# Optimization experiments

Measured on AMD Instinct MI355X. Metric: run time of the kernel, lower is better.

The kernel has to match this reference:

```python
import jax, jax.numpy as jnp
import numpy as np

D_IN = 1024
D_OUT = 1024

def setup_inputs() -> dict:
    key = jax.random.key(0)
    ks = jax.random.split(key, 7)
    s = 1.0 / np.sqrt(D_IN)
    x = jax.random.normal(ks[0], (4, 2048, D_IN), dtype=jnp.float32)
    Wq = jax.random.uniform(ks[1], (D_IN, D_OUT), jnp.float32, -s, s)
    Wk = jax.random.uniform(ks[2], (D_IN, D_OUT), jnp.float32, -s, s)
    Wv = jax.random.uniform(ks[3], (D_IN, D_OUT), jnp.float32, -s, s)
    bq = jax.random.uniform(ks[4], (D_OUT,), jnp.float32, -s, s)
    bk = jax.random.uniform(ks[5], (D_OUT,), jnp.float32, -s, s)
    bv = jax.random.uniform(ks[6], (D_OUT,), jnp.float32, -s, s)
    return {"x": x, "Wq": Wq, "Wk": Wk, "Wv": Wv, "bq": bq, "bk": bk, "bv": bv}

def reference(x, Wq, Wk, Wv, bq, bk, bv):
    # x: [b, n, d_in]
    q = jnp.einsum('bnd,de->bne', x, Wq) + bq
    k = jnp.einsum('bnd,de->bne', x, Wk) + bk
    v = jnp.einsum('bnd,de->bne', x, Wv) + bv
    scale = 1.0 / jnp.sqrt(jnp.asarray(k.shape[-1], dtype=x.dtype))
    scores = jnp.einsum('bqe,bke->bqk', q, k) * scale  # [b, n, n]
    weights = jax.nn.softmax(scores, axis=-1)
    return jnp.einsum('bqk,bke->bqe', weights, v)
```

## Files before the change

kernel.cpp:

```cpp
#include <hip/hip_runtime.h>
#include <cstdint>

typedef __bf16 bf16x8 __attribute__((ext_vector_type(8)));
typedef float f32x16 __attribute__((ext_vector_type(16)));

__device__ __forceinline__ unsigned short f2b(float f) {
    union { float f; uint32_t u; } x; x.f = f;
    uint32_t r = (x.u + 0x7fffu + ((x.u >> 16) & 1u)) >> 16;
    return (unsigned short)r;
}
__device__ __forceinline__ float b2f(unsigned short h) {
    union { float f; uint32_t u; } x; x.u = ((uint32_t)h) << 16;
    return x.f;
}

__global__ __launch_bounds__(256) void convert_x_kernel(const float* __restrict__ x,
                                                        unsigned short* __restrict__ xb) {
    int i = (blockIdx.x * 256 + threadIdx.x) * 4;
    float4 v = *(const float4*)(x + i);
    ushort4 o;
    o.x = f2b(v.x); o.y = f2b(v.y); o.z = f2b(v.z); o.w = f2b(v.w);
    *(ushort4*)(xb + i) = o;
}

__global__ __launch_bounds__(1024) void transpose_w_kernel(const float* __restrict__ Wq,
                                                           const float* __restrict__ Wk,
                                                           const float* __restrict__ Wv,
                                                           unsigned short* __restrict__ Wt) {
    __shared__ float tile[32][33];
    const float* W = (blockIdx.z == 0) ? Wq : (blockIdx.z == 1) ? Wk : Wv;
    int n0 = blockIdx.x * 32, k0 = blockIdx.y * 32;
    int tx = threadIdx.x, ty = threadIdx.y;
    tile[ty][tx] = W[(k0 + ty) * 1024 + n0 + tx];
    __syncthreads();
    Wt[((long)blockIdx.z * 1024 + n0 + ty) * 1024 + k0 + tx] = f2b(tile[tx][ty]);
}

template <int EPI>
__global__ __launch_bounds__(256) void gemm32(const unsigned short* __restrict__ A, int lda, long sA,
                                              const unsigned short* __restrict__ Bm, int ldb, long sB,
                                              void* __restrict__ Cv, long sC, int K,
                                              const float* __restrict__ bq, const float* __restrict__ bk,
                                              const float* __restrict__ bv,
                                              unsigned short* __restrict__ Qb,
                                              unsigned short* __restrict__ Kb,
                                              unsigned short* __restrict__ Vt) {
    __shared__ unsigned short As0[128 * 64];
    __shared__ unsigned short Bs0[128 * 64];
    __shared__ unsigned short As1[128 * 64];
    __shared__ unsigned short Bs1[128 * 64];

    const int tid = threadIdx.x;
    const int wave = tid >> 6, lane = tid & 63;
    const int h = lane >> 5;
    const int l31 = lane & 31;
    const int wm = wave >> 1, wn = wave & 1;
    const long bm = (long)blockIdx.y * 128;
    const long bn = (long)blockIdx.x * 128;

    const unsigned short* Ab = A + (long)blockIdx.z * sA;
    const unsigned short* Bb = Bm + (long)blockIdx.z * sB;

    f32x16 acc[2][2];
#pragma unroll
    for (int mi = 0; mi < 2; ++mi) {
#pragma unroll
        for (int ni = 0; ni < 2; ++ni) {
#pragma unroll
            for (int r = 0; r < 16; ++r) acc[mi][ni][r] = 0.0f;
        }
    }

    const int srow_in = lane >> 3;
    const int cswz = (lane & 7) ^ srow_in;
    const unsigned short* aptr[4];
    const unsigned short* bptr[4];
    int sloff[4];
#pragma unroll
    for (int j = 0; j < 4; ++j) {
        const int row = j * 32 + wave * 8 + srow_in;
        aptr[j] = Ab + (bm + row) * (long)lda + cswz * 8;
        bptr[j] = Bb + (bn + row) * (long)ldb + cswz * 8;
        sloff[j] = (j * 32 + wave * 8) * 64;
    }

    const int arow0 = (wm * 64 + l31) * 64;
    const int brow0 = (wn * 64 + l31) * 64;
    int sw[4];
#pragma unroll
    for (int kh = 0; kh < 4; ++kh)
        sw[kh] = (((2 * kh + h) ^ (lane & 7)) * 8);

#define STAGE(AsB, BsB, kofs)                                                                           \
    do {                                                                                                \
        _Pragma("unroll")                                                                               \
        for (int j = 0; j < 4; ++j) {                                                                   \
            __builtin_amdgcn_global_load_lds(                                                           \
                (const __attribute__((address_space(1))) void*)(aptr[j] + (kofs)),                      \
                (__attribute__((address_space(3))) void*)(&AsB[sloff[j]]), 16, 0, 0);                   \
            __builtin_amdgcn_global_load_lds(                                                           \
                (const __attribute__((address_space(1))) void*)(bptr[j] + (kofs)),                      \
                (__attribute__((address_space(3))) void*)(&BsB[sloff[j]]), 16, 0, 0);                   \
        }                                                                                               \
    } while (0)

#define COMPUTE_T(AsB, BsB)                                                                             \
    do {                                                                                                \
        _Pragma("unroll")                                                                               \
        for (int kp = 0; kp < 2; ++kp) {                                                                \
            bf16x8 af[2][2], bfr[2][2];                                                                 \
            _Pragma("unroll")                                                                           \
            for (int mi = 0; mi < 2; ++mi) {                                                            \
                _Pragma("unroll")                                                                       \
                for (int kk = 0; kk < 2; ++kk) {                                                        \
                    af[mi][kk] = *(const bf16x8*)&AsB[arow0 + mi * 32 * 64 + sw[kp * 2 + kk]];          \
                }                                                                                       \
            }                                                                                           \
            _Pragma("unroll")                                                                           \
            for (int ni = 0; ni < 2; ++ni) {                                                            \
                _Pragma("unroll")                                                                       \
                for (int kk = 0; kk < 2; ++kk) {                                                        \
                    bfr[ni][kk] = *(const bf16x8*)&BsB[brow0 + ni * 32 * 64 + sw[kp * 2 + kk]];         \
                }                                                                                       \
            }                                                                                           \
            _Pragma("unroll")                                                                           \
            for (int kk = 0; kk < 2; ++kk) {                                                            \
                _Pragma("unroll")                                                                       \
                for (int mi = 0; mi < 2; ++mi) {                                                        \
                    _Pragma("unroll")                                                                   \
                    for (int ni = 0; ni < 2; ++ni) {                                                    \
                        acc[mi][ni] = __builtin_amdgcn_mfma_f32_32x32x16_bf16(af[mi][kk], bfr[ni][kk],  \
                                                                              acc[mi][ni], 0, 0, 0);    \
                    }                                                                                   \
                }                                                                                       \
            }                                                                                           \
        }                                                                                               \
    } while (0)

    STAGE(As0, Bs0, 0);

    for (int k0 = 0; k0 < K; k0 += 128) {
        __syncthreads();
        STAGE(As1, Bs1, k0 + 64);
        COMPUTE_T(As0, Bs0);
        __syncthreads();
        if (k0 + 128 < K) STAGE(As0, Bs0, k0 + 128);
        COMPUTE_T(As1, Bs1);
    }

#undef STAGE
#undef COMPUTE_T

#pragma unroll
    for (int mi = 0; mi < 2; ++mi) {
#pragma unroll
        for (int ni = 0; ni < 2; ++ni) {
            const f32x16 a = acc[mi][ni];
            const long col = bn + wn * 64 + ni * 32 + l31;
            const long rowB = bm + wm * 64 + mi * 32 + h * 4;
            if constexpr (EPI == 0) {
                if (col < 1024) {
                    const float bias = bq[col];
#pragma unroll
                    for (int g = 0; g < 4; ++g) {
#pragma unroll
                        for (int r = 0; r < 4; ++r)
                            Qb[(rowB + g * 8 + r) * 1024 + col] = f2b((a[g * 4 + r] + bias) * 0.03125f);
                    }
                } else if (col < 2048) {
                    const float bias = bk[col - 1024];
#pragma unroll
                    for (int g = 0; g < 4; ++g) {
#pragma unroll
                        for (int r = 0; r < 4; ++r)
                            Kb[(rowB + g * 8 + r) * 1024 + (col - 1024)] = f2b(a[g * 4 + r] + bias);
                    }
                } else {
                    const float bias = bv[col - 2048];
#pragma unroll
                    for (int g = 0; g < 4; ++g) {
                        const long row0 = rowB + g * 8;
                        const long batch = row0 >> 11;
                        const int n = (int)(row0 & 2047);
                        ushort4 o;
                        o.x = f2b(a[g * 4 + 0] + bias);
                        o.y = f2b(a[g * 4 + 1] + bias);
                        o.z = f2b(a[g * 4 + 2] + bias);
                        o.w = f2b(a[g * 4 + 3] + bias);
                        *(ushort4*)&Vt[(batch * 1024 + (col - 2048)) * 2048 + n] = o;
                    }
                }
            } else if constexpr (EPI == 1) {
                unsigned short* S = (unsigned short*)Cv + (long)blockIdx.z * sC;
#pragma unroll
                for (int g = 0; g < 4; ++g) {
#pragma unroll
                    for (int r = 0; r < 4; ++r)
                        S[(rowB + g * 8 + r) * 2048 + col] = f2b(a[g * 4 + r]);
                }
            } else {
                float* O = (float*)Cv + (long)blockIdx.z * sC;
#pragma unroll
                for (int g = 0; g < 4; ++g) {
#pragma unroll
                    for (int r = 0; r < 4; ++r)
                        O[(rowB + g * 8 + r) * 1024 + col] = a[g * 4 + r];
                }
            }
        }
    }
}

__global__ __launch_bounds__(256) void softmax_kernel(unsigned short* __restrict__ S) {
    const long row = blockIdx.x;
    unsigned short* p = S + row * 2048;
    const int tid = threadIdx.x;
    const int wave = tid >> 6, lane = tid & 63;

    ushort4 u0 = *(const ushort4*)&p[tid * 8];
    ushort4 u1 = *(const ushort4*)&p[tid * 8 + 4];
    float v[8];
    v[0] = b2f(u0.x); v[1] = b2f(u0.y); v[2] = b2f(u0.z); v[3] = b2f(u0.w);
    v[4] = b2f(u1.x); v[5] = b2f(u1.y); v[6] = b2f(u1.z); v[7] = b2f(u1.w);

    float m = v[0];
#pragma unroll
    for (int j = 1; j < 8; ++j) m = fmaxf(m, v[j]);
#pragma unroll
    for (int off = 32; off; off >>= 1) m = fmaxf(m, __shfl_xor(m, off, 64));
    __shared__ float redm[4];
    __shared__ float reds[4];
    if (lane == 0) redm[wave] = m;
    __syncthreads();
    m = fmaxf(fmaxf(redm[0], redm[1]), fmaxf(redm[2], redm[3]));

    float s = 0.0f;
#pragma unroll
    for (int j = 0; j < 8; ++j) { v[j] = __expf(v[j] - m); s += v[j]; }
#pragma unroll
    for (int off = 32; off; off >>= 1) s += __shfl_xor(s, off, 64);
    if (lane == 0) reds[wave] = s;
    __syncthreads();
    s = reds[0] + reds[1] + reds[2] + reds[3];
    const float inv = 1.0f / s;

    u0.x = f2b(v[0] * inv); u0.y = f2b(v[1] * inv); u0.z = f2b(v[2] * inv); u0.w = f2b(v[3] * inv);
    u1.x = f2b(v[4] * inv); u1.y = f2b(v[5] * inv); u1.z = f2b(v[6] * inv); u1.w = f2b(v[7] * inv);
    *(ushort4*)&p[tid * 8] = u0;
    *(ushort4*)&p[tid * 8 + 4] = u1;
}

extern "C" void kernel_launch(void* const* d_in, const int* in_sizes, int n_in,
                              void* d_out, int out_size, void* d_ws, size_t ws_size,
                              hipStream_t stream) {
    const float* x  = (const float*)d_in[0];
    const float* Wq = (const float*)d_in[1];
    const float* Wk = (const float*)d_in[2];
    const float* Wv = (const float*)d_in[3];
    const float* bq = (const float*)d_in[4];
    const float* bk = (const float*)d_in[5];
    const float* bv = (const float*)d_in[6];
    float* out = (float*)d_out;

    char* ws = (char*)d_ws;
    unsigned short* xb = (unsigned short*)ws; ws += 8192L * 1024 * 2;
    unsigned short* Wt = (unsigned short*)ws; ws += 3072L * 1024 * 2;
    unsigned short* Qb = (unsigned short*)ws; ws += 8192L * 1024 * 2;
    unsigned short* Kb = (unsigned short*)ws; ws += 8192L * 1024 * 2;
    unsigned short* Vt = (unsigned short*)ws; ws += 4L * 1024 * 2048 * 2;
    unsigned short* S  = (unsigned short*)ws; ws += 4L * 2048 * 2048 * 2;

    convert_x_kernel<<<8192, 256, 0, stream>>>(x, xb);
    transpose_w_kernel<<<dim3(32, 32, 3), dim3(32, 32), 0, stream>>>(Wq, Wk, Wv, Wt);
    gemm32<0><<<dim3(24, 64, 1), 256, 0, stream>>>(xb, 1024, 0, Wt, 1024, 0,
                                                   nullptr, 0, 1024, bq, bk, bv, Qb, Kb, Vt);
    gemm32<1><<<dim3(16, 16, 4), 256, 0, stream>>>(Qb, 1024, 2048L * 1024, Kb, 1024, 2048L * 1024,
                                                   S, 2048L * 2048, 1024,
                                                   nullptr, nullptr, nullptr, nullptr, nullptr, nullptr);
    softmax_kernel<<<8192, 256, 0, stream>>>(S);
    gemm32<2><<<dim3(8, 16, 4), 256, 0, stream>>>(S, 2048, 2048L * 2048, Vt, 2048, 2048L * 1024,
                                                  out, 2048L * 1024, 2048,
                                                  nullptr, nullptr, nullptr, nullptr, nullptr, nullptr);
}
```

Before: 261.5 us.

## Add 256x256 tiled MFMA GEMM with LDS double buffering for QKV and scores

Adds a new GEMM kernel with 256x256 output tiles and 512 threads. It loads tiles straight from global memory into LDS with XOR swizzling and double buffering, and splits each tile into four phases so that MFMA 16x16x32 work overlaps with the next loads. It replaces the QKV projection and the Q·K^T score GEMMs, aiming for more operand reuse per byte and better latency hiding. The cost is more LDS (128KB per block, which limits occupancy), a hand-tuned vmcnt schedule that is fragile, and a smaller grid that may underfill the CUs.

After: 294.0 us. 1.12x slower.

```diff
diff --git a/kernel.cpp b/kernel.cpp
--- a/kernel.cpp
+++ b/kernel.cpp
@@ -3,6 +3,7 @@
 
 typedef __bf16 bf16x8 __attribute__((ext_vector_type(8)));
 typedef float f32x16 __attribute__((ext_vector_type(16)));
+typedef float f32x4 __attribute__((ext_vector_type(4)));
 
 __device__ __forceinline__ unsigned short f2b(float f) {
     union { float f; uint32_t u; } x; x.f = f;
@@ -211,6 +212,170 @@
     }
 }
 
+template <int EPI>
+__global__ __launch_bounds__(512, 2) void gemm256(const unsigned short* __restrict__ A, int lda, long sA,
+                                                  const unsigned short* __restrict__ Bm, int ldb, long sB,
+                                                  void* __restrict__ Cv, long sC, int K,
+                                                  const float* __restrict__ bq, const float* __restrict__ bk,
+                                                  const float* __restrict__ bv,
+                                                  unsigned short* __restrict__ Qb,
+                                                  unsigned short* __restrict__ Kb,
+                                                  unsigned short* __restrict__ Vt) {
+    __shared__ __align__(16) unsigned short As_[2][256 * 64];
+    __shared__ __align__(16) unsigned short Bs_[2][256 * 64];
+
+    const int tid = threadIdx.x;
+    const int w = tid >> 6, l = tid & 63;
+    const int wm = w >> 2, wn = w & 3;
+    const long bm = (long)blockIdx.y * 256;
+    const long bn = (long)blockIdx.x * 256;
+    const unsigned short* Ab = A + (long)blockIdx.z * sA;
+    const unsigned short* Bb = Bm + (long)blockIdx.z * sB;
+
+    const int lrow = l >> 3;
+    const int lchunk = (l & 7) ^ lrow;
+    const int fr = l & 15, fg = l >> 4;
+    const int kofs0 = ((fg) ^ (l & 7)) * 8;
+    const int kofs1 = ((4 + fg) ^ (l & 7)) * 8;
+    const int abase = (wm * 128 + fr) * 64;
+    const int bbase = (wn * 64 + fr) * 64;
+
+    f32x4 acc[8][4];
+#pragma unroll
+    for (int mi = 0; mi < 8; ++mi) {
+#pragma unroll
+        for (int ni = 0; ni < 4; ++ni) {
+#pragma unroll
+            for (int r = 0; r < 4; ++r) acc[mi][ni][r] = 0.0f;
+        }
+    }
+
+#define ISSUE_A256(bufi, hh, T)                                                                          \
+    {                                                                                                    \
+        const int kk_ = ((T) * 64 < K) ? (T) * 64 : (K - 64);                                            \
+        _Pragma("unroll")                                                                                \
+        for (int j = 0; j < 2; ++j) {                                                                    \
+            const int rb = (hh) * 64 + j * 128 + w * 8;                                                  \
+            __builtin_amdgcn_global_load_lds(                                                            \
+                (const __attribute__((address_space(1))) void*)(Ab + (bm + rb + lrow) * (long)lda + kk_ + lchunk * 8), \
+                (__attribute__((address_space(3))) void*)(&As_[bufi][rb * 64]), 16, 0, 0);               \
+        }                                                                                                \
+    }
+#define ISSUE_B256(bufi, hh, T)                                                                          \
+    {                                                                                                    \
+        const int kk_ = ((T) * 64 < K) ? (T) * 64 : (K - 64);                                            \
+        _Pragma("unroll")                                                                                \
+        for (int j = 0; j < 2; ++j) {                                                                    \
+            const int rb = (hh) * 32 + (w >> 2) * 64 + (w & 3) * 8 + j * 128;                            \
+            __builtin_amdgcn_global_load_lds(                                                            \
+                (const __attribute__((address_space(1))) void*)(Bb + (bn + rb + lrow) * (long)ldb + kk_ + lchunk * 8), \
+                (__attribute__((address_space(3))) void*)(&Bs_[bufi][rb * 64]), 16, 0, 0);               \
+        }                                                                                                \
+    }
+#define WAITV(n) asm volatile("s_waitcnt vmcnt(" #n ")" ::: "memory")
+
+#define PHASE256(ABUF, BBUF, QM, QN, ISSUE_STMT, WAIT_STMT)                                              \
+    {                                                                                                    \
+        bf16x8 a_[4][2], b_[2][2];                                                                       \
+        _Pragma("unroll")                                                                                \
+        for (int mi = 0; mi < 4; ++mi) {                                                                 \
+            a_[mi][0] = *(const bf16x8*)&(ABUF)[abase + (QM)*4096 + mi * 1024 + kofs0];                  \
+            a_[mi][1] = *(const bf16x8*)&(ABUF)[abase + (QM)*4096 + mi * 1024 + kofs1];                  \
+        }                                                                                                \
+        _Pragma("unroll")                                                                                \
+        for (int ni = 0; ni < 2; ++ni) {                                                                 \
+            b_[ni][0] = *(const bf16x8*)&(BBUF)[bbase + (QN)*2048 + ni * 1024 + kofs0];                  \
+            b_[ni][1] = *(const bf16x8*)&(BBUF)[bbase + (QN)*2048 + ni * 1024 + kofs1];                  \
+        }                                                                                                \
+        ISSUE_STMT;                                                                                      \
+        __builtin_amdgcn_s_barrier();                                                                    \
+        __builtin_amdgcn_sched_barrier(0);                                                               \
+        __builtin_amdgcn_s_setprio(1);                                                                   \
+        _Pragma("unroll")                                                                                \
+        for (int ks = 0; ks < 2; ++ks) {                                                                 \
+            _Pragma("unroll")                                                                            \
+            for (int mi = 0; mi < 4; ++mi) {                                                             \
+                _Pragma("unroll")                                                                        \
+                for (int ni = 0; ni < 2; ++ni) {                                                         \
+                    acc[(QM)*4 + mi][(QN)*2 + ni] = __builtin_amdgcn_mfma_f32_16x16x32_bf16(             \
+                        a_[mi][ks], b_[ni][ks], acc[(QM)*4 + mi][(QN)*2 + ni], 0, 0, 0);                 \
+                }                                                                                        \
+            }                                                                                            \
+        }                                                                                                \
+        __builtin_amdgcn_s_setprio(0);                                                                   \
+        WAIT_STMT;                                                                                       \
+        __builtin_amdgcn_s_barrier();                                                                    \
+        __builtin_amdgcn_sched_barrier(0);                                                               \
+    }
+
+    ISSUE_A256(0, 0, 0);
+    ISSUE_B256(0, 0, 0);
+    ISSUE_A256(0, 1, 0);
+    ISSUE_B256(0, 1, 0);
+    ISSUE_A256(1, 0, 1);
+    ISSUE_B256(1, 0, 1);
+    WAITV(4);
+    __builtin_amdgcn_s_barrier();
+    __builtin_amdgcn_sched_barrier(0);
+
+    const int NT = K >> 6;
+    for (int it = 0; it < NT; it += 2) {
+        PHASE256(As_[0], Bs_[0], 0, 0, ISSUE_A256(1, 1, it + 1), WAITV(6));
+        PHASE256(As_[0], Bs_[0], 0, 1, ISSUE_B256(1, 1, it + 1), ((void)0));
+        PHASE256(As_[0], Bs_[0], 1, 0, ISSUE_A256(0, 0, it + 2), ((void)0));
+        PHASE256(As_[0], Bs_[0], 1, 1, ISSUE_B256(0, 0, it + 2), WAITV(8));
+        PHASE256(As_[1], Bs_[1], 0, 0, ISSUE_A256(0, 1, it + 2), WAITV(6));
+        PHASE256(As_[1], Bs_[1], 0, 1, ISSUE_B256(0, 1, it + 2), ((void)0));
+        PHASE256(As_[1], Bs_[1], 1, 0, ISSUE_A256(1, 0, it + 3), ((void)0));
+        PHASE256(As_[1], Bs_[1], 1, 1, ISSUE_B256(1, 0, it + 3), WAITV(8));
+    }
+
+    asm volatile("s_waitcnt vmcnt(0)" ::: "memory");
+
+#undef ISSUE_A256
+#undef ISSUE_B256
+#undef WAITV
+#undef PHASE256
+
+#pragma unroll
+    for (int mi = 0; mi < 8; ++mi) {
+        const long grow = bm + wm * 128 + mi * 16 + fg * 4;
+#pragma unroll
+        for (int ni = 0; ni < 4; ++ni) {
+            const long gcol = bn + wn * 64 + ni * 16 + fr;
+            const f32x4 a = acc[mi][ni];
+            if constexpr (EPI == 0) {
+                if (gcol < 1024) {
+                    const float bias = bq[gcol];
+#pragma unroll
+                    for (int r = 0; r < 4; ++r)
+                        Qb[(grow + r) * 1024 + gcol] = f2b((a[r] + bias) * 0.03125f);
+                } else if (gcol < 2048) {
+                    const float bias = bk[gcol - 1024];
+#pragma unroll
+                    for (int r = 0; r < 4; ++r)
+                        Kb[(grow + r) * 1024 + (gcol - 1024)] = f2b(a[r] + bias);
+                } else {
+                    const float bias = bv[gcol - 2048];
+                    const long batch = grow >> 11;
+                    const int n = (int)(grow & 2047);
+                    ushort4 o;
+                    o.x = f2b(a[0] + bias);
+                    o.y = f2b(a[1] + bias);
+                    o.z = f2b(a[2] + bias);
+                    o.w = f2b(a[3] + bias);
+                    *(ushort4*)&Vt[(batch * 1024 + (gcol - 2048)) * 2048 + n] = o;
+                }
+            } else {
+                unsigned short* S = (unsigned short*)Cv + (long)blockIdx.z * sC;
+#pragma unroll
+                for (int r = 0; r < 4; ++r)
+                    S[(grow + r) * 2048 + gcol] = f2b(a[r]);
+            }
+        }
+    }
+}
+
 __global__ __launch_bounds__(256) void softmax_kernel(unsigned short* __restrict__ S) {
     const long row = blockIdx.x;
     unsigned short* p = S + row * 2048;
@@ -272,11 +437,11 @@
 
     convert_x_kernel<<<8192, 256, 0, stream>>>(x, xb);
     transpose_w_kernel<<<dim3(32, 32, 3), dim3(32, 32), 0, stream>>>(Wq, Wk, Wv, Wt);
-    gemm32<0><<<dim3(24, 64, 1), 256, 0, stream>>>(xb, 1024, 0, Wt, 1024, 0,
-                                                   nullptr, 0, 1024, bq, bk, bv, Qb, Kb, Vt);
-    gemm32<1><<<dim3(16, 16, 4), 256, 0, stream>>>(Qb, 1024, 2048L * 1024, Kb, 1024, 2048L * 1024,
-                                                   S, 2048L * 2048, 1024,
-                                                   nullptr, nullptr, nullptr, nullptr, nullptr, nullptr);
+    gemm256<0><<<dim3(12, 32, 1), 512, 0, stream>>>(xb, 1024, 0, Wt, 1024, 0,
+                                                    nullptr, 0, 1024, bq, bk, bv, Qb, Kb, Vt);
+    gemm256<1><<<dim3(8, 8, 4), 512, 0, stream>>>(Qb, 1024, 2048L * 1024, Kb, 1024, 2048L * 1024,
+                                                  S, 2048L * 2048, 1024,
+                                                  nullptr, nullptr, nullptr, nullptr, nullptr, nullptr);
     softmax_kernel<<<8192, 256, 0, stream>>>(S);
     gemm32<2><<<dim3(8, 16, 4), 256, 0, stream>>>(S, 2048, 2048L * 2048, Vt, 2048, 2048L * 1024,
                                                   out, 2048L * 1024, 2048,
```
